# Kernel tuning notes

Measured on AMD Instinct MI355X. Metric: run time of the kernel, lower is better.

## Reference

```python
import jax, jax.numpy as jnp
import numpy as np

D_MODEL = 512
NUM_HEADS = 8
NUM_SIGNALS = 8
HEAD_DIM = D_MODEL // NUM_HEADS          # 64
D_H = HEAD_DIM // NUM_SIGNALS            # 8
LN_EPS = 1e-5


def setup_inputs() -> dict:
    key = jax.random.key(0)
    ks = jax.random.split(key, 8)
    B, N, C = 2, 2048, D_MODEL
    s = 1.0 / np.sqrt(C)
    return {
        "x": jax.random.normal(ks[0], (B, N, C), dtype=jnp.float32),
        "mask": jax.random.randint(ks[1], (B, N), 0, 2, dtype=jnp.int32),
        "ln_g": jnp.ones((C,), dtype=jnp.float32),
        "ln_b": jnp.zeros((C,), dtype=jnp.float32),
        "wq": jax.random.normal(ks[2], (C, C), dtype=jnp.float32) * s,
        "bq": jnp.zeros((C,), dtype=jnp.float32),
        "wk": jax.random.normal(ks[3], (C, C), dtype=jnp.float32) * s,
        "bk": jnp.zeros((C,), dtype=jnp.float32),
        "wv": jax.random.normal(ks[4], (C, C), dtype=jnp.float32) * s,
        "bv": jnp.zeros((C,), dtype=jnp.float32),
        "wo": jax.random.normal(ks[5], (C, C), dtype=jnp.float32) * s,
        "bo": jnp.zeros((C,), dtype=jnp.float32),
    }


def reference(x, mask, ln_g, ln_b, wq, bq, wk, bk, wv, bv, wo, bo):
    B, N, C = x.shape
    H, S, dh, hd = NUM_HEADS, NUM_SIGNALS, D_H, HEAD_DIM
    # LayerNorm
    mu = jnp.mean(x, axis=-1, keepdims=True)
    var = jnp.mean(jnp.square(x - mu), axis=-1, keepdims=True)
    xn = (x - mu) * jax.lax.rsqrt(var + LN_EPS) * ln_g + ln_b
    # Projections (torch Linear: y = x @ W.T + b; here weights are stored (in,out))
    q = (xn @ wq + bq).reshape(B, N, H, hd).transpose(0, 2, 1, 3)  # (B,H,N,hd)
    k = (xn @ wk + bk).reshape(B, N, H, hd).transpose(0, 2, 1, 3)
    v = (xn @ wv + bv).reshape(B, N, H, hd).transpose(0, 2, 1, 3)
    # mean over S signals of q_s k_s^T / sqrt(d_h) == full-head contraction / (S*sqrt(d_h))
    scale = 1.0 / (S * np.sqrt(dh))
    avg_logits = jnp.einsum("bhnd,bhmd->bhnm", q, k) * scale  # (B,H,N,N)
    # key-padding mask: (B,N) -> (B,1,1,N)
    avg_logits = jnp.where(mask[:, None, None, :] == 0, -10000.0, avg_logits)
    attn = jax.nn.softmax(avg_logits, axis=-1)
    attn = jnp.nan_to_num(attn)
    out = jnp.einsum("bhnm,bhmd->bhnd", attn, v)  # (B,H,N,hd)
    out = out.transpose(0, 2, 1, 3).reshape(B, N, C)
    return out @ wo + bo
```

## Files before the change

### kernel.cpp

```cpp
#include <hip/hip_runtime.h>
#include <math.h>

#define SEQ_N 2048
#define BATCH 2
#define CDIM 512
#define NHEADS 8
#define MROWS (BATCH * SEQ_N)
#define QKV_N 1536
#define KSPLIT 1536
#define ATTN_SCALE 0.044194173824159216f
#define BH (BATCH * NHEADS)
#define ROWS_ALL (BH * SEQ_N)

typedef __attribute__((ext_vector_type(8))) __bf16 bf16x8;
typedef __attribute__((ext_vector_type(4))) float  f32x4;

static __device__ __forceinline__ unsigned short f2bf(float f) {
    __bf16 h = (__bf16)f;
    return __builtin_bit_cast(unsigned short, h);
}
static __device__ __forceinline__ float bf2f(unsigned short u) {
    return (float)__builtin_bit_cast(__bf16, u);
}

static __device__ __forceinline__ void gll16(const void* g, void* l) {
    __builtin_amdgcn_global_load_lds(
        (const __attribute__((address_space(1))) unsigned int*)g,
        (__attribute__((address_space(3))) unsigned int*)l, 16, 0, 0);
}

__global__ __launch_bounds__(128) void ln_split_kernel(
    const float* __restrict__ x, const float* __restrict__ g,
    const float* __restrict__ bta,
    unsigned short* __restrict__ xn_hi, unsigned short* __restrict__ xn_lo)
{
    int row = blockIdx.x;
    int t = threadIdx.x;
    const float4* xr = (const float4*)(x + (size_t)row * CDIM);
    float4 v = xr[t];
    float s  = v.x + v.y + v.z + v.w;
    float ss = v.x*v.x + v.y*v.y + v.z*v.z + v.w*v.w;
    #pragma unroll
    for (int off = 1; off <= 32; off <<= 1) {
        s  += __shfl_xor(s,  off);
        ss += __shfl_xor(ss, off);
    }
    __shared__ float red[4];
    if ((t & 63) == 0) { red[(t >> 6) * 2] = s; red[(t >> 6) * 2 + 1] = ss; }
    __syncthreads();
    s  = red[0] + red[2];
    ss = red[1] + red[3];
    float mean = s * (1.0f / CDIM);
    float var  = ss * (1.0f / CDIM) - mean * mean;
    float rstd = rsqrtf(var + 1e-5f);
    float4 gv = ((const float4*)g)[t];
    float4 bv = ((const float4*)bta)[t];
    float o[4];
    o[0] = (v.x - mean) * rstd * gv.x + bv.x;
    o[1] = (v.y - mean) * rstd * gv.y + bv.y;
    o[2] = (v.z - mean) * rstd * gv.z + bv.z;
    o[3] = (v.w - mean) * rstd * gv.w + bv.w;
    unsigned int ph[2], pl[2];
    #pragma unroll
    for (int i = 0; i < 2; ++i) {
        unsigned short h0 = f2bf(o[2*i]);
        unsigned short h1 = f2bf(o[2*i+1]);
        unsigned short l0 = f2bf(o[2*i]   - bf2f(h0));
        unsigned short l1 = f2bf(o[2*i+1] - bf2f(h1));
        ph[i] = (unsigned int)h0 | ((unsigned int)h1 << 16);
        pl[i] = (unsigned int)l0 | ((unsigned int)l1 << 16);
    }
    *(uint2*)&xn_hi[(size_t)row * CDIM + t * 4] = make_uint2(ph[0], ph[1]);
    *(uint2*)&xn_lo[(size_t)row * CDIM + t * 4] = make_uint2(pl[0], pl[1]);
}

__global__ __launch_bounds__(256) void wsplit_kernel(
    const float* __restrict__ wq, const float* __restrict__ wk,
    const float* __restrict__ wv, const float* __restrict__ wo,
    unsigned short* __restrict__ BTqkv, unsigned short* __restrict__ BTo)
{
    int m = blockIdx.z;
    const float* W = (m == 0) ? wq : (m == 1) ? wk : (m == 2) ? wv : wo;
    int k0 = blockIdx.y * 64, c0 = blockIdx.x * 64;
    __shared__ float tile[64][68];
    int t = threadIdx.x;
    int r = t >> 4, ch = t & 15;
    #pragma unroll
    for (int i = 0; i < 4; ++i) {
        float4 v = *(const float4*)&W[(size_t)(k0 + r + i*16) * CDIM + c0 + ch*4];
        tile[r + i*16][ch*4 + 0] = v.x; tile[r + i*16][ch*4 + 1] = v.y;
        tile[r + i*16][ch*4 + 2] = v.z; tile[r + i*16][ch*4 + 3] = v.w;
    }
    __syncthreads();
    unsigned short* BT = (m < 3) ? BTqkv : BTo;
    int nbase = (m < 3) ? m * CDIM : 0;
    #pragma unroll
    for (int i = 0; i < 4; ++i) {
        int c  = c0 + r + i*16;
        int kk = k0 + ch*4;
        unsigned int hi2[2], lo2[2];
        #pragma unroll
        for (int half = 0; half < 2; ++half) {
            unsigned short h[2], l[2];
            #pragma unroll
            for (int j = 0; j < 2; ++j) {
                float v = tile[ch*4 + half*2 + j][r + i*16];
                h[j] = f2bf(v);
                l[j] = f2bf(v - bf2f(h[j]));
            }
            hi2[half] = (unsigned int)h[0] | ((unsigned int)h[1] << 16);
            lo2[half] = (unsigned int)l[0] | ((unsigned int)l[1] << 16);
        }
        size_t ro = (size_t)(nbase + c) * KSPLIT;
        *(uint2*)&BT[ro + kk]        = make_uint2(hi2[0], hi2[1]);
        *(uint2*)&BT[ro + 512 + kk]  = make_uint2(lo2[0], lo2[1]);
        *(uint2*)&BT[ro + 1024 + kk] = make_uint2(hi2[0], hi2[1]);
    }
}

template<int BN>
__global__ __launch_bounds__(BN == 128 ? 512 : 256) void gemm_split_kernel(
    const unsigned short* __restrict__ Ahi, const unsigned short* __restrict__ Alo,
    const unsigned short* __restrict__ BT,
    const float* __restrict__ b0, const float* __restrict__ b1,
    const float* __restrict__ b2,
    unsigned short* __restrict__ outb, float* __restrict__ outf)
{
    constexpr int NT  = (BN == 128) ? 512 : 256;
    constexpr int ACH = 1024 / NT;
    constexpr int BCH = (BN * 8) / NT;
    __shared__ unsigned short As[128 * 64];
    __shared__ unsigned short Bs[BN * 64];
    int tid = threadIdx.x;
    int l = tid & 63, w = tid >> 6;
    int am = (BN == 128) ? (w >> 2) : (w >> 1);
    int an = (BN == 128) ? (w & 3)  : (w & 1);
    int m0 = blockIdx.y * 128, n0 = blockIdx.x * BN;

    f32x4 acc[4][2];
    #pragma unroll
    for (int fm = 0; fm < 4; ++fm)
        #pragma unroll
        for (int fn = 0; fn < 2; ++fn)
            acc[fm][fn] = (f32x4){0.f, 0.f, 0.f, 0.f};

    for (int kt = 0; kt < 24; ++kt) {
        int kp  = kt * 64;
        int seg = kp >> 9;
        const unsigned short* Asrc = (seg < 2) ? Ahi : Alo;
        int ac0 = kp & 511;
        __syncthreads();
        #pragma unroll
        for (int i = 0; i < ACH; ++i) {
            int c = tid + i * NT;
            int row = c >> 3, c8 = c & 7;
            gll16(Asrc + (size_t)(m0 + row) * CDIM + ac0 + c8 * 8, &As[c * 8]);
        }
        #pragma unroll
        for (int i = 0; i < BCH; ++i) {
            int c = tid + i * NT;
            int row = c >> 3, c8 = c & 7;
            gll16(BT + (size_t)(n0 + row) * KSPLIT + kp + c8 * 8, &Bs[c * 8]);
        }
        __syncthreads();
        #pragma unroll
        for (int kc = 0; kc < 2; ++kc) {
            bf16x8 af[4], bfr[2];
            #pragma unroll
            for (int fm = 0; fm < 4; ++fm)
                af[fm] = *(const bf16x8*)&As[(am*64 + fm*16 + (l & 15)) * 64 + kc*32 + (l >> 4) * 8];
            #pragma unroll
            for (int fn = 0; fn < 2; ++fn)
                bfr[fn] = *(const bf16x8*)&Bs[(an*32 + fn*16 + (l & 15)) * 64 + kc*32 + (l >> 4) * 8];
            #pragma unroll
            for (int fm = 0; fm < 4; ++fm)
                #pragma unroll
                for (int fn = 0; fn < 2; ++fn)
                    acc[fm][fn] = __builtin_amdgcn_mfma_f32_16x16x32_bf16(
                        af[fm], bfr[fn], acc[fm][fn], 0, 0, 0);
        }
    }
    #pragma unroll
    for (int fm = 0; fm < 4; ++fm)
        #pragma unroll
        for (int fn = 0; fn < 2; ++fn)
            #pragma unroll
            for (int r = 0; r < 4; ++r) {
                int row = m0 + am*64 + fm*16 + (l >> 4) * 4 + r;
                int col = n0 + an*32 + fn*16 + (l & 15);
                float v = acc[fm][fn][r];
                if (outb) {
                    float bias = (col < 512) ? b0[col]
                               : (col < 1024) ? b1[col - 512] : b2[col - 1024];
                    outb[(size_t)row * QKV_N + col] = f2bf(v + bias);
                } else {
                    outf[(size_t)row * CDIM + col] = v + b0[col];
                }
            }
}

__global__ __launch_bounds__(256) void attn_kernel(
    const unsigned short* __restrict__ qkv, const int* __restrict__ maskp,
    float* __restrict__ Opart, float* __restrict__ mpart, float* __restrict__ lpart,
    unsigned short* __restrict__ ao_hi, unsigned short* __restrict__ ao_lo)
{
    __shared__ unsigned short Ks[64 * 72];
    __shared__ unsigned short VTs[64 * 72];
    __shared__ unsigned short Ps[4][16 * 72];
    __shared__ float mskf[64];

    int tid = threadIdx.x, l = tid & 63, w = tid >> 6;
    int bh = blockIdx.x;
    int b = bh >> 3, head = bh & 7;
    int q0 = blockIdx.y * 64;
    int kvlen = SEQ_N / gridDim.z;
    int kvbeg = blockIdx.z * kvlen;
    size_t brow = (size_t)b * SEQ_N;
    const unsigned short* Qb = qkv + head * 64;
    const unsigned short* Kb = qkv + 512 + head * 64;
    const unsigned short* Vb = qkv + 1024 + head * 64;

    bf16x8 qf[2];
    {
        int qrow = q0 + w * 16 + (l & 15);
        #pragma unroll
        for (int kc = 0; kc < 2; ++kc)
            qf[kc] = *(const bf16x8*)&Qb[(brow + qrow) * QKV_N + kc*32 + (l >> 4) * 8];
    }

    float m_i[4], l_i[4];
    f32x4 o[4];
    #pragma unroll
    for (int r = 0; r < 4; ++r) { m_i[r] = -1e30f; l_i[r] = 0.f; }
    #pragma unroll
    for (int nb = 0; nb < 4; ++nb) o[nb] = (f32x4){0.f, 0.f, 0.f, 0.f};

    for (int kv0 = kvbeg; kv0 < kvbeg + kvlen; kv0 += 64) {
        __syncthreads();
        #pragma unroll
        for (int i = 0; i < 2; ++i) {
            int c = tid + i * 256;
            int row = c >> 3, c8 = c & 7;
            *(uint4*)&Ks[row * 72 + c8 * 8] =
                *(const uint4*)&Kb[(brow + kv0 + row) * QKV_N + c8 * 8];
        }
        #pragma unroll
        for (int i = 0; i < 2; ++i) {
            int c = tid + i * 256;
            int row = c >> 3, c8 = c & 7;
            uint4 vv = *(const uint4*)&Vb[(brow + kv0 + row) * QKV_N + c8 * 8];
            const unsigned short* pv = (const unsigned short*)&vv;
            int swc = ((row >> 3) ^ c8) & 7;
            #pragma unroll
            for (int j = 0; j < 8; ++j)
                VTs[(c8 * 8 + j) * 72 + swc * 8 + (row & 7)] = pv[j];
        }
        if (tid < 64) mskf[tid] = (float)maskp[b * SEQ_N + kv0 + tid];
        __syncthreads();

        f32x4 s[4];
        #pragma unroll
        for (int nb = 0; nb < 4; ++nb) s[nb] = (f32x4){0.f, 0.f, 0.f, 0.f};
        #pragma unroll
        for (int kc = 0; kc < 2; ++kc)
            #pragma unroll
            for (int nb = 0; nb < 4; ++nb) {
                bf16x8 kf = *(const bf16x8*)&Ks[(nb*16 + (l & 15)) * 72 + kc*32 + (l >> 4) * 8];
                s[nb] = __builtin_amdgcn_mfma_f32_16x16x32_bf16(qf[kc], kf, s[nb], 0, 0, 0);
            }

        #pragma unroll
        for (int nb = 0; nb < 4; ++nb) {
            float mk = mskf[nb * 16 + (l & 15)];
            #pragma unroll
            for (int r = 0; r < 4; ++r)
                s[nb][r] = (mk != 0.f) ? s[nb][r] * ATTN_SCALE : -10000.f;
        }

        #pragma unroll
        for (int r = 0; r < 4; ++r) {
            float rm = fmaxf(fmaxf(s[0][r], s[1][r]), fmaxf(s[2][r], s[3][r]));
            #pragma unroll
            for (int off = 1; off < 16; off <<= 1)
                rm = fmaxf(rm, __shfl_xor(rm, off));
            float mnew  = fmaxf(m_i[r], rm);
            float alpha = __expf(m_i[r] - mnew);
            float p[4], rs = 0.f;
            #pragma unroll
            for (int nb = 0; nb < 4; ++nb) { p[nb] = __expf(s[nb][r] - mnew); rs += p[nb]; }
            #pragma unroll
            for (int off = 1; off < 16; off <<= 1)
                rs += __shfl_xor(rs, off);
            l_i[r] = l_i[r] * alpha + rs;
            m_i[r] = mnew;
            #pragma unroll
            for (int nb = 0; nb < 4; ++nb) o[nb][r] *= alpha;
            int prow = (l >> 4) * 4 + r;
            #pragma unroll
            for (int nb = 0; nb < 4; ++nb)
                Ps[w][prow * 72 + nb * 16 + (l & 15)] = f2bf(p[nb]);
        }

        #pragma unroll
        for (int kc = 0; kc < 2; ++kc) {
            bf16x8 pf = *(const bf16x8*)&Ps[w][(l & 15) * 72 + kc*32 + (l >> 4) * 8];
            int kb = kc * 4 + (l >> 4);
            #pragma unroll
            for (int nb = 0; nb < 4; ++nb) {
                int d = nb * 16 + (l & 15);
                bf16x8 vf = *(const bf16x8*)&VTs[d * 72 + ((kb ^ (d >> 3)) & 7) * 8];
                o[nb] = __builtin_amdgcn_mfma_f32_16x16x32_bf16(pf, vf, o[nb], 0, 0, 0);
            }
        }
    }

    if (Opart) {
        int part = blockIdx.z * BH + bh;
        #pragma unroll
        for (int r = 0; r < 4; ++r) {
            int row = q0 + w * 16 + (l >> 4) * 4 + r;
            size_t rbase = ((size_t)part * SEQ_N + row) * 64;
            #pragma unroll
            for (int nb = 0; nb < 4; ++nb)
                Opart[rbase + nb * 16 + (l & 15)] = o[nb][r];
            if ((l & 15) == 0) {
                mpart[(size_t)part * SEQ_N + row] = m_i[r];
                lpart[(size_t)part * SEQ_N + row] = l_i[r];
            }
        }
    } else {
        #pragma unroll
        for (int r = 0; r < 4; ++r) {
            float invl = 1.f / l_i[r];
            int row = q0 + w * 16 + (l >> 4) * 4 + r;
            #pragma unroll
            for (int nb = 0; nb < 4; ++nb) {
                float v = o[nb][r] * invl;
                unsigned short h  = f2bf(v);
                unsigned short lo = f2bf(v - bf2f(h));
                size_t idx = (brow + row) * (size_t)CDIM + head * 64 + nb * 16 + (l & 15);
                ao_hi[idx] = h;
                ao_lo[idx] = lo;
            }
        }
    }
}

__global__ __launch_bounds__(256) void combine_kernel(
    const float* __restrict__ Opart, const float* __restrict__ mpart,
    const float* __restrict__ lpart, int S,
    unsigned short* __restrict__ ao_hi, unsigned short* __restrict__ ao_lo)
{
    int t = threadIdx.x;
    int row = blockIdx.x * 32 + (t >> 3);
    int d0 = (t & 7) * 8;
    float ms = -3.0e38f;
    for (int s = 0; s < S; ++s)
        ms = fmaxf(ms, mpart[(size_t)s * ROWS_ALL + row]);
    float L = 0.f;
    float acc[8] = {0.f,0.f,0.f,0.f,0.f,0.f,0.f,0.f};
    for (int s = 0; s < S; ++s) {
        float wgt = __expf(mpart[(size_t)s * ROWS_ALL + row] - ms);
        L = fmaf(lpart[(size_t)s * ROWS_ALL + row], wgt, L);
        const float4* op = (const float4*)&Opart[((size_t)s * ROWS_ALL + row) * 64 + d0];
        float4 a = op[0], c = op[1];
        acc[0] = fmaf(a.x, wgt, acc[0]); acc[1] = fmaf(a.y, wgt, acc[1]);
        acc[2] = fmaf(a.z, wgt, acc[2]); acc[3] = fmaf(a.w, wgt, acc[3]);
        acc[4] = fmaf(c.x, wgt, acc[4]); acc[5] = fmaf(c.y, wgt, acc[5]);
        acc[6] = fmaf(c.z, wgt, acc[6]); acc[7] = fmaf(c.w, wgt, acc[7]);
    }
    float inv = 1.f / L;
    int bh = row >> 11, n = row & 2047;
    int b = bh >> 3, h = bh & 7;
    size_t oidx = ((size_t)(b * SEQ_N + n)) * CDIM + h * 64 + d0;
    unsigned short hs[8], ls[8];
    #pragma unroll
    for (int j = 0; j < 8; ++j) {
        float v = acc[j] * inv;
        hs[j] = f2bf(v);
        ls[j] = f2bf(v - bf2f(hs[j]));
    }
    *(uint4*)&ao_hi[oidx] = *(uint4*)hs;
    *(uint4*)&ao_lo[oidx] = *(uint4*)ls;
}

extern "C" void kernel_launch(void* const* d_in, const int* in_sizes, int n_in,
                              void* d_out, int out_size, void* d_ws, size_t ws_size,
                              hipStream_t stream) {
    const float* x    = (const float*)d_in[0];
    const int*   mask = (const int*)  d_in[1];
    const float* ln_g = (const float*)d_in[2];
    const float* ln_b = (const float*)d_in[3];
    const float* wq   = (const float*)d_in[4];
    const float* bq   = (const float*)d_in[5];
    const float* wk   = (const float*)d_in[6];
    const float* bk   = (const float*)d_in[7];
    const float* wv   = (const float*)d_in[8];
    const float* bv   = (const float*)d_in[9];
    const float* wo   = (const float*)d_in[10];
    const float* bo   = (const float*)d_in[11];
    float* out = (float*)d_out;

    unsigned short* xn_hi = (unsigned short*)d_ws;
    unsigned short* xn_lo = xn_hi + (size_t)MROWS * CDIM;
    unsigned short* BTqkv = xn_lo + (size_t)MROWS * CDIM;
    unsigned short* BTo   = BTqkv + (size_t)QKV_N * KSPLIT;
    unsigned short* qkvb  = BTo   + (size_t)CDIM * KSPLIT;
    unsigned short* ao_hi = qkvb  + (size_t)MROWS * QKV_N;
    unsigned short* ao_lo = ao_hi + (size_t)MROWS * CDIM;
    unsigned short* ws_end = ao_lo + (size_t)MROWS * CDIM;

    size_t base_bytes = (size_t)((char*)ws_end - (char*)d_ws);
    const size_t part_bytes = (size_t)ROWS_ALL * (64 + 2) * 4;
    int S = 1;
    if (base_bytes + 4 * part_bytes <= ws_size) S = 4;
    else if (base_bytes + 2 * part_bytes <= ws_size) S = 2;

    float* Opart = (float*)ws_end;
    float* mpart = Opart + (size_t)S * ROWS_ALL * 64;
    float* lpart = mpart + (size_t)S * ROWS_ALL;

    ln_split_kernel<<<MROWS, 128, 0, stream>>>(x, ln_g, ln_b, xn_hi, xn_lo);
    wsplit_kernel<<<dim3(8, 8, 4), 256, 0, stream>>>(wq, wk, wv, wo, BTqkv, BTo);

    gemm_split_kernel<128><<<dim3(QKV_N / 128, MROWS / 128), 512, 0, stream>>>(
        xn_hi, xn_lo, BTqkv, bq, bk, bv, qkvb, nullptr);

    if (S > 1) {
        attn_kernel<<<dim3(BH, SEQ_N / 64, S), 256, 0, stream>>>(
            qkvb, mask, Opart, mpart, lpart, nullptr, nullptr);
        combine_kernel<<<ROWS_ALL / 32, 256, 0, stream>>>(
            Opart, mpart, lpart, S, ao_hi, ao_lo);
    } else {
        attn_kernel<<<dim3(BH, SEQ_N / 64, 1), 256, 0, stream>>>(
            qkvb, mask, nullptr, nullptr, nullptr, ao_hi, ao_lo);
    }

    gemm_split_kernel<64><<<dim3(CDIM / 64, MROWS / 128), 256, 0, stream>>>(
        ao_hi, ao_lo, BTo, bo, nullptr, nullptr, nullptr, out);
}
```

Baseline: 244.4 us.

## Enlarge attention query tile, use exp2 softmax with MFMA row sums, rebalance GEMM warps

The attention kernel now runs 512 threads per block covering 128 query rows, so each K/V tile loaded into shared memory serves twice as many queries. Scale and mask are pre-multiplied by log2(e) so softmax uses exp2f. The row-sum shuffle reduction is replaced by an extra MFMA of P against a vector of ones. The QKV GEMM switches from 512 to 256 threads, so each warp covers 64 columns and holds more accumulators. The combine kernel uses exp2f to match. The risks are lower occupancy and more register pressure, and the row sums are now taken from bf16-rounded P values.

```diff
diff --git a/kernel.cpp b/kernel.cpp
--- a/kernel.cpp
+++ b/kernel.cpp
@@ -9,6 +9,9 @@
 #define QKV_N 1536
 #define KSPLIT 1536
 #define ATTN_SCALE 0.044194173824159216f
+#define LOG2E 1.4426950408889634f
+#define SC2 (ATTN_SCALE * LOG2E)
+#define MASK2 (-10000.0f * LOG2E)
 #define BH (BATCH * NHEADS)
 #define ROWS_ALL (BH * SEQ_N)
 
@@ -119,29 +122,28 @@
 }
 
 template<int BN>
-__global__ __launch_bounds__(BN == 128 ? 512 : 256) void gemm_split_kernel(
+__global__ __launch_bounds__(256) void gemm_split_kernel(
     const unsigned short* __restrict__ Ahi, const unsigned short* __restrict__ Alo,
     const unsigned short* __restrict__ BT,
     const float* __restrict__ b0, const float* __restrict__ b1,
     const float* __restrict__ b2,
     unsigned short* __restrict__ outb, float* __restrict__ outf)
 {
-    constexpr int NT  = (BN == 128) ? 512 : 256;
-    constexpr int ACH = 1024 / NT;
-    constexpr int BCH = (BN * 8) / NT;
+    constexpr int FN  = BN / 32;
+    constexpr int WNS = BN / 2;
+    constexpr int BCH = (BN * 8) / 256;
     __shared__ unsigned short As[128 * 64];
     __shared__ unsigned short Bs[BN * 64];
     int tid = threadIdx.x;
     int l = tid & 63, w = tid >> 6;
-    int am = (BN == 128) ? (w >> 2) : (w >> 1);
-    int an = (BN == 128) ? (w & 3)  : (w & 1);
+    int am = w >> 1, an = w & 1;
     int m0 = blockIdx.y * 128, n0 = blockIdx.x * BN;
 
-    f32x4 acc[4][2];
+    f32x4 acc[4][FN];
     #pragma unroll
     for (int fm = 0; fm < 4; ++fm)
         #pragma unroll
-        for (int fn = 0; fn < 2; ++fn)
+        for (int fn = 0; fn < FN; ++fn)
             acc[fm][fn] = (f32x4){0.f, 0.f, 0.f, 0.f};
 
     for (int kt = 0; kt < 24; ++kt) {
@@ -151,31 +153,31 @@
         int ac0 = kp & 511;
         __syncthreads();
         #pragma unroll
-        for (int i = 0; i < ACH; ++i) {
-            int c = tid + i * NT;
+        for (int i = 0; i < 4; ++i) {
+            int c = tid + i * 256;
             int row = c >> 3, c8 = c & 7;
             gll16(Asrc + (size_t)(m0 + row) * CDIM + ac0 + c8 * 8, &As[c * 8]);
         }
         #pragma unroll
         for (int i = 0; i < BCH; ++i) {
-            int c = tid + i * NT;
+            int c = tid + i * 256;
             int row = c >> 3, c8 = c & 7;
             gll16(BT + (size_t)(n0 + row) * KSPLIT + kp + c8 * 8, &Bs[c * 8]);
         }
         __syncthreads();
         #pragma unroll
         for (int kc = 0; kc < 2; ++kc) {
-            bf16x8 af[4], bfr[2];
+            bf16x8 af[4], bfr[FN];
             #pragma unroll
             for (int fm = 0; fm < 4; ++fm)
                 af[fm] = *(const bf16x8*)&As[(am*64 + fm*16 + (l & 15)) * 64 + kc*32 + (l >> 4) * 8];
             #pragma unroll
-            for (int fn = 0; fn < 2; ++fn)
-                bfr[fn] = *(const bf16x8*)&Bs[(an*32 + fn*16 + (l & 15)) * 64 + kc*32 + (l >> 4) * 8];
+            for (int fn = 0; fn < FN; ++fn)
+                bfr[fn] = *(const bf16x8*)&Bs[(an*WNS + fn*16 + (l & 15)) * 64 + kc*32 + (l >> 4) * 8];
             #pragma unroll
             for (int fm = 0; fm < 4; ++fm)
                 #pragma unroll
-                for (int fn = 0; fn < 2; ++fn)
+                for (int fn = 0; fn < FN; ++fn)
                     acc[fm][fn] = __builtin_amdgcn_mfma_f32_16x16x32_bf16(
                         af[fm], bfr[fn], acc[fm][fn], 0, 0, 0);
         }
@@ -183,11 +185,11 @@
     #pragma unroll
     for (int fm = 0; fm < 4; ++fm)
         #pragma unroll
-        for (int fn = 0; fn < 2; ++fn)
+        for (int fn = 0; fn < FN; ++fn)
             #pragma unroll
             for (int r = 0; r < 4; ++r) {
                 int row = m0 + am*64 + fm*16 + (l >> 4) * 4 + r;
-                int col = n0 + an*32 + fn*16 + (l & 15);
+                int col = n0 + an*WNS + fn*16 + (l & 15);
                 float v = acc[fm][fn][r];
                 if (outb) {
                     float bias = (col < 512) ? b0[col]
@@ -199,20 +201,20 @@
             }
 }
 
-__global__ __launch_bounds__(256) void attn_kernel(
+__global__ __launch_bounds__(512) void attn_kernel(
     const unsigned short* __restrict__ qkv, const int* __restrict__ maskp,
     float* __restrict__ Opart, float* __restrict__ mpart, float* __restrict__ lpart,
     unsigned short* __restrict__ ao_hi, unsigned short* __restrict__ ao_lo)
 {
     __shared__ unsigned short Ks[64 * 72];
     __shared__ unsigned short VTs[64 * 72];
-    __shared__ unsigned short Ps[4][16 * 72];
+    __shared__ unsigned short Ps[8][16 * 72];
     __shared__ float mskf[64];
 
     int tid = threadIdx.x, l = tid & 63, w = tid >> 6;
     int bh = blockIdx.x;
     int b = bh >> 3, head = bh & 7;
-    int q0 = blockIdx.y * 64;
+    int q0 = blockIdx.y * 128;
     int kvlen = SEQ_N / gridDim.z;
     int kvbeg = blockIdx.z * kvlen;
     size_t brow = (size_t)b * SEQ_N;
@@ -220,6 +222,9 @@
     const unsigned short* Kb = qkv + 512 + head * 64;
     const unsigned short* Vb = qkv + 1024 + head * 64;
 
+    const __bf16 one_bf = (__bf16)1.0f;
+    bf16x8 onesf = {one_bf, one_bf, one_bf, one_bf, one_bf, one_bf, one_bf, one_bf};
+
     bf16x8 qf[2];
     {
         int qrow = q0 + w * 16 + (l & 15);
@@ -228,26 +233,23 @@
             qf[kc] = *(const bf16x8*)&Qb[(brow + qrow) * QKV_N + kc*32 + (l >> 4) * 8];
     }
 
-    float m_i[4], l_i[4];
-    f32x4 o[4];
-    #pragma unroll
-    for (int r = 0; r < 4; ++r) { m_i[r] = -1e30f; l_i[r] = 0.f; }
+    float m_i[4];
+    f32x4 o[4], osum;
+    #pragma unroll
+    for (int r = 0; r < 4; ++r) m_i[r] = -1e30f;
+    osum = (f32x4){0.f, 0.f, 0.f, 0.f};
     #pragma unroll
     for (int nb = 0; nb < 4; ++nb) o[nb] = (f32x4){0.f, 0.f, 0.f, 0.f};
 
     for (int kv0 = kvbeg; kv0 < kvbeg + kvlen; kv0 += 64) {
         __syncthreads();
-        #pragma unroll
-        for (int i = 0; i < 2; ++i) {
-            int c = tid + i * 256;
-            int row = c >> 3, c8 = c & 7;
+        {
+            int row = tid >> 3, c8 = tid & 7;
             *(uint4*)&Ks[row * 72 + c8 * 8] =
                 *(const uint4*)&Kb[(brow + kv0 + row) * QKV_N + c8 * 8];
         }
-        #pragma unroll
-        for (int i = 0; i < 2; ++i) {
-            int c = tid + i * 256;
-            int row = c >> 3, c8 = c & 7;
+        {
+            int row = tid >> 3, c8 = tid & 7;
             uint4 vv = *(const uint4*)&Vb[(brow + kv0 + row) * QKV_N + c8 * 8];
             const unsigned short* pv = (const unsigned short*)&vv;
             int swc = ((row >> 3) ^ c8) & 7;
@@ -274,7 +276,7 @@
             float mk = mskf[nb * 16 + (l & 15)];
             #pragma unroll
             for (int r = 0; r < 4; ++r)
-                s[nb][r] = (mk != 0.f) ? s[nb][r] * ATTN_SCALE : -10000.f;
+                s[nb][r] = (mk != 0.f) ? s[nb][r] * SC2 : MASK2;
         }
 
         #pragma unroll
@@ -284,26 +286,22 @@
             for (int off = 1; off < 16; off <<= 1)
                 rm = fmaxf(rm, __shfl_xor(rm, off));
             float mnew  = fmaxf(m_i[r], rm);
-            float alpha = __expf(m_i[r] - mnew);
-            float p[4], rs = 0.f;
-            #pragma unroll
-            for (int nb = 0; nb < 4; ++nb) { p[nb] = __expf(s[nb][r] - mnew); rs += p[nb]; }
-            #pragma unroll
-            for (int off = 1; off < 16; off <<= 1)
-                rs += __shfl_xor(rs, off);
-            l_i[r] = l_i[r] * alpha + rs;
+            float alpha = exp2f(m_i[r] - mnew);
             m_i[r] = mnew;
-            #pragma unroll
-            for (int nb = 0; nb < 4; ++nb) o[nb][r] *= alpha;
             int prow = (l >> 4) * 4 + r;
             #pragma unroll
-            for (int nb = 0; nb < 4; ++nb)
-                Ps[w][prow * 72 + nb * 16 + (l & 15)] = f2bf(p[nb]);
+            for (int nb = 0; nb < 4; ++nb) {
+                float p = exp2f(s[nb][r] - mnew);
+                Ps[w][prow * 72 + nb * 16 + (l & 15)] = f2bf(p);
+                o[nb][r] *= alpha;
+            }
+            osum[r] *= alpha;
         }
 
         #pragma unroll
         for (int kc = 0; kc < 2; ++kc) {
             bf16x8 pf = *(const bf16x8*)&Ps[w][(l & 15) * 72 + kc*32 + (l >> 4) * 8];
+            osum = __builtin_amdgcn_mfma_f32_16x16x32_bf16(pf, onesf, osum, 0, 0, 0);
             int kb = kc * 4 + (l >> 4);
             #pragma unroll
             for (int nb = 0; nb < 4; ++nb) {
@@ -325,13 +323,13 @@
                 Opart[rbase + nb * 16 + (l & 15)] = o[nb][r];
             if ((l & 15) == 0) {
                 mpart[(size_t)part * SEQ_N + row] = m_i[r];
-                lpart[(size_t)part * SEQ_N + row] = l_i[r];
+                lpart[(size_t)part * SEQ_N + row] = osum[r];
             }
         }
     } else {
         #pragma unroll
         for (int r = 0; r < 4; ++r) {
-            float invl = 1.f / l_i[r];
+            float invl = 1.f / osum[r];
             int row = q0 + w * 16 + (l >> 4) * 4 + r;
             #pragma unroll
             for (int nb = 0; nb < 4; ++nb) {
@@ -360,7 +358,7 @@
     float L = 0.f;
     float acc[8] = {0.f,0.f,0.f,0.f,0.f,0.f,0.f,0.f};
     for (int s = 0; s < S; ++s) {
-        float wgt = __expf(mpart[(size_t)s * ROWS_ALL + row] - ms);
+        float wgt = exp2f(mpart[(size_t)s * ROWS_ALL + row] - ms);
         L = fmaf(lpart[(size_t)s * ROWS_ALL + row], wgt, L);
         const float4* op = (const float4*)&Opart[((size_t)s * ROWS_ALL + row) * 64 + d0];
         float4 a = op[0], c = op[1];
@@ -423,16 +421,16 @@
     ln_split_kernel<<<MROWS, 128, 0, stream>>>(x, ln_g, ln_b, xn_hi, xn_lo);
     wsplit_kernel<<<dim3(8, 8, 4), 256, 0, stream>>>(wq, wk, wv, wo, BTqkv, BTo);
 
-    gemm_split_kernel<128><<<dim3(QKV_N / 128, MROWS / 128), 512, 0, stream>>>(
+    gemm_split_kernel<128><<<dim3(QKV_N / 128, MROWS / 128), 256, 0, stream>>>(
         xn_hi, xn_lo, BTqkv, bq, bk, bv, qkvb, nullptr);
 
     if (S > 1) {
-        attn_kernel<<<dim3(BH, SEQ_N / 64, S), 256, 0, stream>>>(
+        attn_kernel<<<dim3(BH, SEQ_N / 128, S), 512, 0, stream>>>(
             qkvb, mask, Opart, mpart, lpart, nullptr, nullptr);
         combine_kernel<<<ROWS_ALL / 32, 256, 0, stream>>>(
             Opart, mpart, lpart, S, ao_hi, ao_lo);
     } else {
-        attn_kernel<<<dim3(BH, SEQ_N / 64, 1), 256, 0, stream>>>(
+        attn_kernel<<<dim3(BH, SEQ_N / 128, 1), 512, 0, stream>>>(
             qkvb, mask, nullptr, nullptr, nullptr, ao_hi, ao_lo);
     }
 
```

Result: faster. 226.7 us (-7.2%).
